# Kernel optimization log

Hardware: AMD Instinct MI355X
Metric: run time of the kernel (lower is better)

## Reference

```python
import jax, jax.numpy as jnp
import numpy as np

NEIGHBOR_RATE = 0.1  # neighbor_rate init arg
LEAKY_SLOPE = 0.2
NEG_INF = -1.0e9


def setup_inputs() -> dict:
    key = jax.random.key(0)
    k1, k2, k3, k4 = jax.random.split(key, 4)
    B, N, Din, H, hd = 4, 2048, 128, 4, 32  # output_dim = H*hd = 128
    h = jax.random.normal(k1, (B, N, Din), jnp.float32)
    adj = jax.random.uniform(k2, (B, N, N), jnp.float32)
    # stacked per-head params: W[k] in [Din, hd], a[k] in [2*hd]
    w_bound = 1.0 / np.sqrt(Din)
    a_bound = 1.0 / np.sqrt(2 * hd)
    W = jax.random.uniform(k3, (H, Din, hd), jnp.float32, -w_bound, w_bound)
    a = jax.random.uniform(k4, (H, 2 * hd), jnp.float32, -a_bound, a_bound)
    return {"h": h, "adj": adj, "W": W, "a": a}


def reference(h, adj, W, a):
    B, N, _ = h.shape
    H, _, hd = W.shape
    k = int(NEIGHBOR_RATE * N)  # num_neighbors
    # Wh: [B,H,N,hd]
    Wh = jnp.einsum('bnf,hfd->bhnd', h, W)
    # cat([Wh_i, Wh_j]) @ a  ==  Wh_i @ a[:hd] + Wh_j @ a[hd:] (broadcast trick)
    s_i = jnp.einsum('bhnd,hd->bhn', Wh, a[:, :hd])
    s_j = jnp.einsum('bhnd,hd->bhn', Wh, a[:, hd:])
    e = jax.nn.leaky_relu(s_i[..., :, None] + s_j[..., None, :], LEAKY_SLOPE)  # [B,H,N,N]
    # top-k mask along last (neighbor) axis, built by scatter like torch .scatter_
    _, idx = jax.lax.top_k(e, k)  # [B,H,N,k]
    row_mask = lambda i: jnp.zeros((N,), jnp.bool_).at[i].set(True)
    mask = jax.vmap(row_mask)(idx.reshape(-1, k)).reshape(e.shape)
    masked = jnp.where(mask, e, NEG_INF)
    attn = jax.nn.softmax(masked, axis=-1) * adj[:, None]  # [B,H,N,N]
    hp = jnp.einsum('bhnm,bhmd->bhnd', attn, Wh)
    # concat heads on feature dim -> [B,N,H*hd]
    return hp.transpose(0, 2, 1, 3).reshape(B, N, H * hd)
```

## Files before the change

### kernel.cpp

```cpp
#include <hip/hip_runtime.h>
#include <hip/hip_bf16.h>
#include <cmath>

#define BB 4
#define NN 2048
#define DIN 128
#define HH 4
#define HD 32
#define KSEL 204
#define BH (BB*HH)
#define KPAD 256
#define KST 264

typedef __attribute__((ext_vector_type(8))) short short8;
typedef __attribute__((ext_vector_type(4))) short short4v;
typedef __attribute__((ext_vector_type(4))) float float4v;

static __device__ inline short f2bf(float x) {
    __hip_bfloat16 b = __float2bfloat16(x);
    return __builtin_bit_cast(short, b);
}

__global__ __launch_bounds__(256) void hs_kernel(const float* __restrict__ h,
                                                 const float* __restrict__ W,
                                                 const float* __restrict__ a,
                                                 short* __restrict__ hbf,
                                                 float* __restrict__ si, float* __restrict__ sj) {
    int g = blockIdx.x;
    int bh = g >> 3, chunk = g & 7;
    int b = bh >> 2, hh = bh & 3;
    int t = threadIdx.x;
    {
        const float4* src = (const float4*)h + (size_t)g * 2048;
        short4v* dst = (short4v*)hbf + (size_t)g * 2048;
#pragma unroll
        for (int q = 0; q < 8; ++q) {
            float4 x = src[q * 256 + t];
            short4v r;
            r[0] = f2bf(x.x); r[1] = f2bf(x.y); r[2] = f2bf(x.z); r[3] = f2bf(x.w);
            dst[q * 256 + t] = r;
        }
    }
    __shared__ float w1[128], w2[128];
    {
        int f = t & 127, half = t >> 7;
        const float* Wp = W + (size_t)hh * (DIN * HD) + f * HD;
        const float* ap = a + hh * 64 + half * 32;
        float acc = 0.f;
#pragma unroll
        for (int d = 0; d < 32; ++d) acc += Wp[d] * ap[d];
        if (half == 0) w1[f] = acc; else w2[f] = acc;
    }
    __syncthreads();
    int n = chunk * 256 + t;
    const float4* hr = (const float4*)(h + ((size_t)b * NN + n) * DIN);
    float s1 = 0.f, s2 = 0.f;
#pragma unroll 8
    for (int q = 0; q < 32; ++q) {
        float4 x = hr[q];
        s1 += x.x * w1[q*4] + x.y * w1[q*4+1] + x.z * w1[q*4+2] + x.w * w1[q*4+3];
        s2 += x.x * w2[q*4] + x.y * w2[q*4+1] + x.z * w2[q*4+2] + x.w * w2[q*4+3];
    }
    int o = bh * NN + n;
    si[o] = s1; sj[o] = s2;
}

__global__ __launch_bounds__(256) void wh_kernel(const short* __restrict__ hbf,
                                                 const float* __restrict__ W,
                                                 short* __restrict__ Whg) {
    int bh = blockIdx.x >> 4, rtile = blockIdx.x & 15;
    int b = bh >> 2, hh = bh & 3;
    __shared__ short WT[32][136];
    int t = threadIdx.x;
    for (int e = t; e < 32 * 128; e += 256) {
        int n = e >> 7, k = e & 127;
        WT[n][k] = f2bf(W[(size_t)hh * (DIN * HD) + k * HD + n]);
    }
    __syncthreads();
    int w = t >> 6, lane = t & 63, mr = lane & 15, quad = lane >> 4;
    int row_base = rtile * 128;
#pragma unroll
    for (int q = 0; q < 4; ++q) {
        int tt = w * 4 + q;
        int rt = tt >> 1, ct = tt & 1;
        int row0 = row_base + rt * 16;
        const short* hrow = hbf + ((size_t)b * NN + row0 + mr) * DIN + quad * 8;
        float4v acc = {0.f, 0.f, 0.f, 0.f};
#pragma unroll
        for (int ks = 0; ks < 4; ++ks) {
            short8 afr = *(const short8*)(hrow + ks * 32);
            short8 bfr = *(const short8*)&WT[ct * 16 + mr][ks * 32 + quad * 8];
            acc = __builtin_amdgcn_mfma_f32_16x16x32_bf16(afr, bfr, acc, 0, 0, 0);
        }
#pragma unroll
        for (int r = 0; r < 4; ++r) {
            int rowg = row0 + quad * 4 + r;
            Whg[((size_t)bh * NN + rowg) * HD + ct * 16 + mr] = f2bf(acc[r]);
        }
    }
}

__global__ __launch_bounds__(1024) void select_kernel(
        const float* __restrict__ sj, const short* __restrict__ Whg,
        int* __restrict__ idxsel, float* __restrict__ sjsel,
        float* __restrict__ sjmax, short* __restrict__ Whsel) {
    int bh = blockIdx.x;
    int t = threadIdx.x, lane = t & 63, w = t >> 6;
    __shared__ float sv[NN];
    __shared__ int hist16[16][256];
    __shared__ int binInfo[2];
    __shared__ int wtot[4];
    __shared__ int wtotg[16], wtote[16], woffg[16], woffe[16];
    __shared__ float wmax[16];
    __shared__ int idxLDS[KSEL];

    const float* s = sj + (size_t)bh * NN;
    int j0 = t * 2;
    float x0 = s[j0], x1 = s[j0 + 1];
    sv[j0] = x0; sv[j0 + 1] = x1;
    unsigned u0 = __builtin_bit_cast(unsigned, x0);
    unsigned u1 = __builtin_bit_cast(unsigned, x1);
    u0 = (u0 & 0x80000000u) ? ~u0 : (u0 | 0x80000000u);
    u1 = (u1 & 0x80000000u) ? ~u1 : (u1 | 0x80000000u);
    float lmax = fmaxf(x0, x1);
#pragma unroll
    for (int off = 32; off >= 1; off >>= 1) lmax = fmaxf(lmax, __shfl_xor(lmax, off));
    if (lane == 0) wmax[w] = lmax;
    __syncthreads();
    if (t == 0) {
        float m = wmax[0];
#pragma unroll
        for (int i = 1; i < 16; ++i) m = fmaxf(m, wmax[i]);
        sjmax[bh] = m;
    }

    unsigned prefix = 0;
    int need = KSEL;
#pragma unroll
    for (int shift = 24; shift >= 0; shift -= 8) {
        ((int*)hist16)[t] = 0; ((int*)hist16)[t + 1024] = 0;
        ((int*)hist16)[t + 2048] = 0; ((int*)hist16)[t + 3072] = 0;
        __syncthreads();
        unsigned hmask = (shift < 24) ? (0xFFFFFFFFu << (shift + 8)) : 0u;
        if (((u0 ^ prefix) & hmask) == 0) atomicAdd(&hist16[w][(u0 >> shift) & 255], 1);
        if (((u1 ^ prefix) & hmask) == 0) atomicAdd(&hist16[w][(u1 >> shift) & 255], 1);
        __syncthreads();
        int sc = 0, hv = 0, bb = 0;
        if (t < 256) {
            bb = 255 - t;
            hv = 0;
#pragma unroll
            for (int i = 0; i < 16; ++i) hv += hist16[i][bb];
            sc = hv;
#pragma unroll
            for (int off = 1; off < 64; off <<= 1) {
                int u = __shfl_up(sc, off);
                if (lane >= off) sc += u;
            }
            if (lane == 63) wtot[w] = sc;
        }
        __syncthreads();
        if (t < 256) {
            int woffset = 0;
#pragma unroll
            for (int i = 0; i < 4; ++i) woffset += (i < w) ? wtot[i] : 0;
            int incl = sc + woffset;
            int excl = incl - hv;
            if (incl >= need && excl < need) {
                binInfo[0] = bb;
                binInfo[1] = excl;
            }
        }
        __syncthreads();
        prefix |= ((unsigned)binInfo[0]) << shift;
        need -= binInfo[1];
        __syncthreads();
    }
    unsigned T = prefix;
    int n_gt = KSEL - need;

    int cg = (u0 > T ? 1 : 0) + (u1 > T ? 1 : 0);
    int ce = (u0 == T ? 1 : 0) + (u1 == T ? 1 : 0);
    int sg = cg, se = ce;
#pragma unroll
    for (int off = 1; off < 64; off <<= 1) {
        int ug = __shfl_up(sg, off), ue = __shfl_up(se, off);
        if (lane >= off) { sg += ug; se += ue; }
    }
    if (lane == 63) { wtotg[w] = sg; wtote[w] = se; }
    __syncthreads();
    if (t == 0) {
        int rg = 0, re = 0;
#pragma unroll
        for (int i = 0; i < 16; ++i) {
            woffg[i] = rg; rg += wtotg[i];
            woffe[i] = re; re += wtote[i];
        }
    }
    __syncthreads();
    int pg = woffg[w] + sg - cg;
    int te = woffe[w] + se - ce;
    {
        unsigned kk[2] = {u0, u1};
#pragma unroll
        for (int r = 0; r < 2; ++r) {
            int j = j0 + r;
            if (kk[r] > T) {
                idxsel[bh * KSEL + pg] = j;
                sjsel[bh * KSEL + pg] = sv[j];
                idxLDS[pg] = j;
                pg++;
            } else if (kk[r] == T) {
                if (te < need) {
                    int pos = n_gt + te;
                    idxsel[bh * KSEL + pos] = j;
                    sjsel[bh * KSEL + pos] = sv[j];
                    idxLDS[pos] = j;
                }
                te++;
            }
        }
    }
    __syncthreads();
    for (int e = t; e < HD * KPAD; e += 1024) {
        int d = e >> 8, jj = e & 255;
        short v = 0;
        if (jj < KSEL) v = Whg[((size_t)bh * NN + idxLDS[jj]) * HD + d];
        Whsel[((size_t)bh * HD + d) * KPAD + jj] = v;
    }
}

__global__ __launch_bounds__(256) void attn2_kernel(
        const float* __restrict__ adj, const float* __restrict__ si,
        const int* __restrict__ idxsel, const float* __restrict__ sjsel,
        const float* __restrict__ sjmax, const short* __restrict__ Whsel,
        float* __restrict__ out) {
    int b = blockIdx.x >> 7;
    int tile = blockIdx.x & 127;
    __shared__ float adjbuf[4][NN];
    __shared__ short PSb[HH][16][KST];
    __shared__ int   idxS[HH][KPAD];
    __shared__ float sjS[HH][KPAD];
    __shared__ float invZS[HH][16];
    __shared__ float smaxS[HH];
    int t = threadIdx.x, w = t >> 6, lane = t & 63;
    int mr = lane & 15, quad = lane >> 4;

    for (int e = t; e < HH * KPAD; e += 256) {
        int hh = e >> 8, jj = e & 255;
        bool v = jj < KSEL;
        idxS[hh][jj] = v ? idxsel[(b * HH + hh) * KSEL + jj] : 0;
        sjS[hh][jj]  = v ? sjsel[(b * HH + hh) * KSEL + jj] : -1e30f;
    }
    if (t < HH) smaxS[t] = sjmax[b * HH + t];

    short8 bfr[2][8];
    {
        const short* wp = Whsel + (size_t)((b * HH + w) * HD) * KPAD;
#pragma unroll
        for (int ni = 0; ni < 2; ++ni)
#pragma unroll
            for (int ks = 0; ks < 8; ++ks)
                bfr[ni][ks] = *(const short8*)(wp + (size_t)(ni * 16 + mr) * KPAD + ks * 32 + quad * 8);
    }

    int i0 = tile * 16;
    const float* adjb = adj + (size_t)b * NN * NN;
    {
        const float4* src = (const float4*)(adjb + (size_t)i0 * NN);
        float4* dst = (float4*)adjbuf;
#pragma unroll
        for (int q = 0; q < 8; ++q)
            dst[q * 256 + t] = src[q * 256 + t];
    }
    __syncthreads();

    int bh = b * HH + w;
    float smax = smaxS[w];
    for (int s = 0; s < 4; ++s) {
#pragma unroll
        for (int r = 0; r < 4; ++r) {
            int i_loc = s * 4 + r;
            int i = i0 + i_loc;
            float siv = si[(size_t)bh * NN + i];
            float m = siv + smax;
            m = (m >= 0.f) ? m : 0.2f * m;
            float z = 0.f;
            short* prow = &PSb[w][i_loc][0];
#pragma unroll
            for (int k = 0; k < 2; ++k) {
                int jj = k * 128 + lane * 2;
                int ja = idxS[w][jj], jb = idxS[w][jj + 1];
                float ava = adjbuf[r][ja], avb = adjbuf[r][jb];
                float ea = siv + sjS[w][jj];
                float eb = siv + sjS[w][jj + 1];
                ea = (ea >= 0.f) ? ea : 0.2f * ea;
                eb = (eb >= 0.f) ? eb : 0.2f * eb;
                float ca = __expf(ea - m);
                float cb = __expf(eb - m);
                z += ca + cb;
                short2 p;
                p.x = f2bf(ca * ava);
                p.y = f2bf(cb * avb);
                *(short2*)&prow[jj] = p;
            }
#pragma unroll
            for (int off = 32; off >= 1; off >>= 1) z += __shfl_xor(z, off);
            if (lane == 0) invZS[w][i_loc] = 1.0f / z;
        }
        if (s < 3) {
            __syncthreads();
            const float4* src = (const float4*)(adjb + (size_t)(i0 + (s + 1) * 4) * NN);
            float4* dst = (float4*)adjbuf;
#pragma unroll
            for (int q = 0; q < 8; ++q)
                dst[q * 256 + t] = src[q * 256 + t];
            __syncthreads();
        }
    }
#pragma unroll
    for (int ni = 0; ni < 2; ++ni) {
        float4v acc = {0.f, 0.f, 0.f, 0.f};
#pragma unroll
        for (int ks = 0; ks < 8; ++ks) {
            short8 afr = *(const short8*)&PSb[w][mr][ks * 32 + quad * 8];
            acc = __builtin_amdgcn_mfma_f32_16x16x32_bf16(afr, bfr[ni][ks], acc, 0, 0, 0);
        }
#pragma unroll
        for (int r = 0; r < 4; ++r) {
            int i_loc = quad * 4 + r;
            int d = ni * 16 + mr;
            out[((size_t)(b * NN + i0 + i_loc)) * (HH * HD) + w * HD + d] =
                acc[r] * invZS[w][i_loc];
        }
    }
}

extern "C" void kernel_launch(void* const* d_in, const int* in_sizes, int n_in,
                              void* d_out, int out_size, void* d_ws, size_t ws_size,
                              hipStream_t stream) {
    const float* h   = (const float*)d_in[0];
    const float* adj = (const float*)d_in[1];
    const float* W   = (const float*)d_in[2];
    const float* a   = (const float*)d_in[3];
    float* out = (float*)d_out;

    float* si     = (float*)d_ws;
    float* sj     = si + (size_t)BH * NN;
    float* sjsel  = sj + (size_t)BH * NN;
    float* sjmax  = sjsel + (size_t)BH * KSEL;
    int*   idxsel = (int*)(sjmax + 16);
    short* hbf    = (short*)(idxsel + (size_t)BH * KSEL);
    short* Whg    = hbf + (size_t)BB * NN * DIN;
    short* Whsel  = Whg + (size_t)BH * NN * HD;

    hs_kernel<<<BH * 8, 256, 0, stream>>>(h, W, a, hbf, si, sj);
    wh_kernel<<<BH * 16, 256, 0, stream>>>(hbf, W, Whg);
    select_kernel<<<BH, 1024, 0, stream>>>(sj, Whg, idxsel, sjsel, sjmax, Whsel);
    attn2_kernel<<<BB * 128, 256, 0, stream>>>(adj, si, idxsel, sjsel, sjmax, Whsel, out);
}
```

Before: 133.4 us.

## Fuse score and Wh projection into select kernel, computing Wh only for selected columns

Removes the hs and wh kernels. The select kernel now computes the per-node attention scores si/sj itself from h, and computes the Wh projection with MFMA only for the 204 selected neighbor rows instead of all 2048. This cuts two launches, the bf16 copy of h and the full Wh buffer round trip through global memory. The cost is that only 16 blocks (one per batch-head) now read all of h for the score dot products, with each thread reading two full rows serially, so this phase has far less parallelism.

```diff
diff --git a/kernel.cpp b/kernel.cpp
--- a/kernel.cpp
+++ b/kernel.cpp
@@ -21,92 +21,17 @@
     return __builtin_bit_cast(short, b);
 }
 
-__global__ __launch_bounds__(256) void hs_kernel(const float* __restrict__ h,
-                                                 const float* __restrict__ W,
-                                                 const float* __restrict__ a,
-                                                 short* __restrict__ hbf,
-                                                 float* __restrict__ si, float* __restrict__ sj) {
-    int g = blockIdx.x;
-    int bh = g >> 3, chunk = g & 7;
-    int b = bh >> 2, hh = bh & 3;
-    int t = threadIdx.x;
-    {
-        const float4* src = (const float4*)h + (size_t)g * 2048;
-        short4v* dst = (short4v*)hbf + (size_t)g * 2048;
-#pragma unroll
-        for (int q = 0; q < 8; ++q) {
-            float4 x = src[q * 256 + t];
-            short4v r;
-            r[0] = f2bf(x.x); r[1] = f2bf(x.y); r[2] = f2bf(x.z); r[3] = f2bf(x.w);
-            dst[q * 256 + t] = r;
-        }
-    }
-    __shared__ float w1[128], w2[128];
-    {
-        int f = t & 127, half = t >> 7;
-        const float* Wp = W + (size_t)hh * (DIN * HD) + f * HD;
-        const float* ap = a + hh * 64 + half * 32;
-        float acc = 0.f;
-#pragma unroll
-        for (int d = 0; d < 32; ++d) acc += Wp[d] * ap[d];
-        if (half == 0) w1[f] = acc; else w2[f] = acc;
-    }
-    __syncthreads();
-    int n = chunk * 256 + t;
-    const float4* hr = (const float4*)(h + ((size_t)b * NN + n) * DIN);
-    float s1 = 0.f, s2 = 0.f;
-#pragma unroll 8
-    for (int q = 0; q < 32; ++q) {
-        float4 x = hr[q];
-        s1 += x.x * w1[q*4] + x.y * w1[q*4+1] + x.z * w1[q*4+2] + x.w * w1[q*4+3];
-        s2 += x.x * w2[q*4] + x.y * w2[q*4+1] + x.z * w2[q*4+2] + x.w * w2[q*4+3];
-    }
-    int o = bh * NN + n;
-    si[o] = s1; sj[o] = s2;
-}
-
-__global__ __launch_bounds__(256) void wh_kernel(const short* __restrict__ hbf,
-                                                 const float* __restrict__ W,
-                                                 short* __restrict__ Whg) {
-    int bh = blockIdx.x >> 4, rtile = blockIdx.x & 15;
-    int b = bh >> 2, hh = bh & 3;
-    __shared__ short WT[32][136];
-    int t = threadIdx.x;
-    for (int e = t; e < 32 * 128; e += 256) {
-        int n = e >> 7, k = e & 127;
-        WT[n][k] = f2bf(W[(size_t)hh * (DIN * HD) + k * HD + n]);
-    }
-    __syncthreads();
-    int w = t >> 6, lane = t & 63, mr = lane & 15, quad = lane >> 4;
-    int row_base = rtile * 128;
-#pragma unroll
-    for (int q = 0; q < 4; ++q) {
-        int tt = w * 4 + q;
-        int rt = tt >> 1, ct = tt & 1;
-        int row0 = row_base + rt * 16;
-        const short* hrow = hbf + ((size_t)b * NN + row0 + mr) * DIN + quad * 8;
-        float4v acc = {0.f, 0.f, 0.f, 0.f};
-#pragma unroll
-        for (int ks = 0; ks < 4; ++ks) {
-            short8 afr = *(const short8*)(hrow + ks * 32);
-            short8 bfr = *(const short8*)&WT[ct * 16 + mr][ks * 32 + quad * 8];
-            acc = __builtin_amdgcn_mfma_f32_16x16x32_bf16(afr, bfr, acc, 0, 0, 0);
-        }
-#pragma unroll
-        for (int r = 0; r < 4; ++r) {
-            int rowg = row0 + quad * 4 + r;
-            Whg[((size_t)bh * NN + rowg) * HD + ct * 16 + mr] = f2bf(acc[r]);
-        }
-    }
-}
-
 __global__ __launch_bounds__(1024) void select_kernel(
-        const float* __restrict__ sj, const short* __restrict__ Whg,
+        const float* __restrict__ h, const float* __restrict__ W,
+        const float* __restrict__ a, float* __restrict__ si,
         int* __restrict__ idxsel, float* __restrict__ sjsel,
         float* __restrict__ sjmax, short* __restrict__ Whsel) {
     int bh = blockIdx.x;
+    int b = bh >> 2, hh = bh & 3;
     int t = threadIdx.x, lane = t & 63, w = t >> 6;
     __shared__ float sv[NN];
+    __shared__ float w1[128], w2[128];
+    __shared__ short WT[32][136];
     __shared__ int hist16[16][256];
     __shared__ int binInfo[2];
     __shared__ int wtot[4];
@@ -114,15 +39,44 @@
     __shared__ float wmax[16];
     __shared__ int idxLDS[KSEL];
 
-    const float* s = sj + (size_t)bh * NN;
+    if (t < 256) {
+        int f = t & 127, half = t >> 7;
+        const float* Wp = W + (size_t)hh * (DIN * HD) + f * HD;
+        const float* ap = a + hh * 64 + half * 32;
+        float acc = 0.f;
+#pragma unroll
+        for (int d = 0; d < 32; ++d) acc += Wp[d] * ap[d];
+        if (half == 0) w1[f] = acc; else w2[f] = acc;
+    }
+    for (int e = t; e < 32 * 128; e += 1024) {
+        int n = e >> 7, k = e & 127;
+        WT[n][k] = f2bf(W[(size_t)hh * (DIN * HD) + k * HD + n]);
+    }
+    __syncthreads();
+
     int j0 = t * 2;
-    float x0 = s[j0], x1 = s[j0 + 1];
-    sv[j0] = x0; sv[j0 + 1] = x1;
-    unsigned u0 = __builtin_bit_cast(unsigned, x0);
-    unsigned u1 = __builtin_bit_cast(unsigned, x1);
+    float s1a = 0.f, s2a = 0.f, s1b = 0.f, s2b = 0.f;
+    {
+        const float4* hr0 = (const float4*)(h + ((size_t)b * NN + j0) * DIN);
+        const float4* hr1 = hr0 + (DIN / 4);
+#pragma unroll 8
+        for (int q = 0; q < 32; ++q) {
+            float4 x = hr0[q];
+            s1a += x.x * w1[q*4] + x.y * w1[q*4+1] + x.z * w1[q*4+2] + x.w * w1[q*4+3];
+            s2a += x.x * w2[q*4] + x.y * w2[q*4+1] + x.z * w2[q*4+2] + x.w * w2[q*4+3];
+            float4 y = hr1[q];
+            s1b += y.x * w1[q*4] + y.y * w1[q*4+1] + y.z * w1[q*4+2] + y.w * w1[q*4+3];
+            s2b += y.x * w2[q*4] + y.y * w2[q*4+1] + y.z * w2[q*4+2] + y.w * w2[q*4+3];
+        }
+    }
+    si[(size_t)bh * NN + j0]     = s1a;
+    si[(size_t)bh * NN + j0 + 1] = s1b;
+    sv[j0] = s2a; sv[j0 + 1] = s2b;
+    unsigned u0 = __builtin_bit_cast(unsigned, s2a);
+    unsigned u1 = __builtin_bit_cast(unsigned, s2b);
     u0 = (u0 & 0x80000000u) ? ~u0 : (u0 | 0x80000000u);
     u1 = (u1 & 0x80000000u) ? ~u1 : (u1 | 0x80000000u);
-    float lmax = fmaxf(x0, x1);
+    float lmax = fmaxf(s2a, s2b);
 #pragma unroll
     for (int off = 32; off >= 1; off >>= 1) lmax = fmaxf(lmax, __shfl_xor(lmax, off));
     if (lane == 0) wmax[w] = lmax;
@@ -222,11 +176,37 @@
         }
     }
     __syncthreads();
-    for (int e = t; e < HD * KPAD; e += 1024) {
-        int d = e >> 8, jj = e & 255;
-        short v = 0;
-        if (jj < KSEL) v = Whg[((size_t)bh * NN + idxLDS[jj]) * HD + d];
-        Whsel[((size_t)bh * HD + d) * KPAD + jj] = v;
+
+    {
+        int mr = lane & 15, quad = lane >> 4;
+        int jjp = w * 16 + mr;
+        bool valid = jjp < KSEL;
+        const float* hrow = h + ((size_t)b * NN + (valid ? idxLDS[jjp] : 0)) * DIN + quad * 8;
+        float4v acc0 = {0.f, 0.f, 0.f, 0.f};
+        float4v acc1 = {0.f, 0.f, 0.f, 0.f};
+#pragma unroll
+        for (int ks = 0; ks < 4; ++ks) {
+            short8 afr;
+            if (valid) {
+                float4 xa = *(const float4*)(hrow + ks * 32);
+                float4 xb = *(const float4*)(hrow + ks * 32 + 4);
+                afr[0] = f2bf(xa.x); afr[1] = f2bf(xa.y); afr[2] = f2bf(xa.z); afr[3] = f2bf(xa.w);
+                afr[4] = f2bf(xb.x); afr[5] = f2bf(xb.y); afr[6] = f2bf(xb.z); afr[7] = f2bf(xb.w);
+            } else {
+                afr = (short8){0, 0, 0, 0, 0, 0, 0, 0};
+            }
+            short8 b0 = *(const short8*)&WT[mr][ks * 32 + quad * 8];
+            short8 b1 = *(const short8*)&WT[16 + mr][ks * 32 + quad * 8];
+            acc0 = __builtin_amdgcn_mfma_f32_16x16x32_bf16(afr, b0, acc0, 0, 0, 0);
+            acc1 = __builtin_amdgcn_mfma_f32_16x16x32_bf16(afr, b1, acc1, 0, 0, 0);
+        }
+        short4v o0, o1;
+#pragma unroll
+        for (int r = 0; r < 4; ++r) { o0[r] = f2bf(acc0[r]); o1[r] = f2bf(acc1[r]); }
+        size_t base = (size_t)bh * HD * KPAD;
+        int jjs = w * 16 + quad * 4;
+        *(short4v*)&Whsel[base + (size_t)mr * KPAD + jjs] = o0;
+        *(short4v*)&Whsel[base + (size_t)(16 + mr) * KPAD + jjs] = o1;
     }
 }
 
@@ -346,16 +326,11 @@
     float* out = (float*)d_out;
 
     float* si     = (float*)d_ws;
-    float* sj     = si + (size_t)BH * NN;
-    float* sjsel  = sj + (size_t)BH * NN;
+    float* sjsel  = si + (size_t)BH * NN;
     float* sjmax  = sjsel + (size_t)BH * KSEL;
     int*   idxsel = (int*)(sjmax + 16);
-    short* hbf    = (short*)(idxsel + (size_t)BH * KSEL);
-    short* Whg    = hbf + (size_t)BB * NN * DIN;
-    short* Whsel  = Whg + (size_t)BH * NN * HD;
-
-    hs_kernel<<<BH * 8, 256, 0, stream>>>(h, W, a, hbf, si, sj);
-    wh_kernel<<<BH * 16, 256, 0, stream>>>(hbf, W, Whg);
-    select_kernel<<<BH, 1024, 0, stream>>>(sj, Whg, idxsel, sjsel, sjmax, Whsel);
+    short* Whsel  = (short*)(idxsel + (size_t)BH * KSEL);
+
+    select_kernel<<<BH, 1024, 0, stream>>>(h, W, a, si, idxsel, sjsel, sjmax, Whsel);
     attn2_kernel<<<BB * 128, 256, 0, stream>>>(adj, si, idxsel, sjsel, sjmax, Whsel, out);
 }
```

Result: slower. 165.6 us (+24.1%).
